# Performance work log

Measured on AMD Instinct MI355X. Metric: run time of the kernel, lower is better.

The kernel has to match this reference:

```python
import jax, jax.numpy as jnp
import numpy as np

N = 50000   # total nodes
E = 100000  # total edges
F = 64      # input node features
H = 128     # hidden_dim
HEADS = 4
B = 64      # number of graphs in the batch
S = 512     # num_stations
LC = 8      # num_line_colors


def setup_inputs() -> dict:
    key = jax.random.key(0)
    ks = jax.random.split(key, 40)
    w = lambda i, shape: (jax.random.normal(ks[i], shape, jnp.float32) * 0.02)
    inp = {
        'node_features': jax.random.normal(ks[0], (N, F), jnp.float32),
        'edge_index': jax.random.randint(ks[1], (2, E), 0, N),
        'batch': jnp.sort(jax.random.randint(ks[2], (N,), 0, B)),
        # initial projection F -> H
        'Wp': w(3, (F, H)), 'bp': w(4, (H,)),
        # TransformerConv 1: in H, out H, heads HEADS (concat)
        'Wq1': w(5, (H, HEADS * H)), 'bq1': w(6, (HEADS * H,)),
        'Wk1': w(7, (H, HEADS * H)), 'bk1': w(8, (HEADS * H,)),
        'Wv1': w(9, (H, HEADS * H)), 'bv1': w(10, (HEADS * H,)),
        'Ws1': w(11, (H, HEADS * H)), 'bs1': w(12, (HEADS * H,)),
        # TransformerConv 2: in HEADS*H, out H, heads 1
        'Wq2': w(13, (HEADS * H, H)), 'bq2': w(14, (H,)),
        'Wk2': w(15, (HEADS * H, H)), 'bk2': w(16, (H,)),
        'Wv2': w(17, (HEADS * H, H)), 'bv2': w(18, (H,)),
        'Ws2': w(19, (HEADS * H, H)), 'bs2': w(20, (H,)),
        # output heads
        'crW': w(21, (H, 1)),  'crb': w(22, (1,)),
        'hlW': w(23, (H, 4)),  'hlb': w(24, (4,)),
        'mtW': w(25, (H, 3)),  'mtb': w(26, (3,)),
        'p1W': w(27, (H, S)),  'p1b': w(28, (S,)),
        'p2W': w(29, (H, S)),  'p2b': w(30, (S,)),
        'dtW': w(31, (H, S)),  'dtb': w(32, (S,)),
        'slW': w(33, (H, LC)), 'slb': w(34, (LC,)),
    }
    return inp


def transformer_conv(x, src, dst, Wq, bq, Wk, bk, Wv, bv, Ws, bs, heads, out_ch):
    # PyG TransformerConv (beta=False, concat=True, root_weight=True):
    #   alpha_ij = softmax_j( (W_q x_i) . (W_k x_j) / sqrt(d) ) over in-edges of i
    #   out_i    = sum_j alpha_ij * (W_v x_j)  (concat heads) + W_skip x_i
    n = x.shape[0]
    q = (x @ Wq + bq).reshape(n, heads, out_ch)
    k = (x @ Wk + bk).reshape(n, heads, out_ch)
    v = (x @ Wv + bv).reshape(n, heads, out_ch)
    scores = jnp.sum(q[dst] * k[src], axis=-1) / jnp.sqrt(jnp.float32(out_ch))  # [E,heads]
    m = jax.ops.segment_max(scores, dst, num_segments=n)                        # per-target max
    e = jnp.exp(scores - m[dst])
    denom = jax.ops.segment_sum(e, dst, num_segments=n)
    alpha = e / (denom[dst] + 1e-16)                                            # [E,heads]
    out = jax.ops.segment_sum(alpha[:, :, None] * v[src], dst, num_segments=n)  # [N,heads,out]
    return out.reshape(n, heads * out_ch) + (x @ Ws + bs)


def reference(node_features, edge_index, batch, Wp, bp,
              Wq1, bq1, Wk1, bk1, Wv1, bv1, Ws1, bs1,
              Wq2, bq2, Wk2, bk2, Wv2, bv2, Ws2, bs2,
              crW, crb, hlW, hlb, mtW, mtb, p1W, p1b, p2W, p2b, dtW, dtb, slW, slb):
    src, dst = edge_index[0], edge_index[1]
    h = jax.nn.relu(node_features @ Wp + bp)
    h = jax.nn.relu(transformer_conv(h, src, dst, Wq1, bq1, Wk1, bk1, Wv1, bv1, Ws1, bs1, HEADS, H))
    h = jax.nn.relu(transformer_conv(h, src, dst, Wq2, bq2, Wk2, bk2, Wv2, bv2, Ws2, bs2, 1, H))
    # global mean pool over graphs
    counts = jax.ops.segment_sum(jnp.ones((h.shape[0],), h.dtype), batch, num_segments=B)
    g = jax.ops.segment_sum(h, batch, num_segments=B) / jnp.maximum(counts, 1.0)[:, None]  # [B,H]
    value = g @ crW + crb
    return (value,
            g @ hlW + hlb,
            g @ mtW + mtb,
            g @ p1W + p1b,
            g @ p2W + p2b,
            g @ dtW + dtb,
            g @ slW + slb)
```

## Files before the change

kernel.cpp:

```cpp
#include <hip/hip_runtime.h>
#include <hip/hip_bf16.h>

#define NN 50000
#define EE 100000
#define FF 64
#define HH 128
#define HEADS 4
#define BB 64
#define SS 512
#define LCC 8
#define DEGCAP 32

__device__ __forceinline__ float b2f(ushort u) {
    return __uint_as_float(((unsigned)u) << 16);
}
__device__ __forceinline__ ushort f2b(float f) {
    unsigned u = __float_as_uint(f);
    unsigned r = (u + 0x7FFFu + ((u >> 16) & 1u)) >> 16;
    return (ushort)r;
}
__device__ __forceinline__ uint f2b_pk(float a, float b) {
    __hip_bfloat162 h = __float22bfloat162_rn(make_float2(a, b));
    return *reinterpret_cast<uint*>(&h);
}

__device__ __forceinline__ uint f2fp8x4(float a, float b, float c, float d) {
    int r = __builtin_amdgcn_cvt_pk_fp8_f32(a, b, 0, false);
    r = __builtin_amdgcn_cvt_pk_fp8_f32(c, d, r, true);
    return (uint)r;
}
__device__ __forceinline__ void fp8x4(uint u, float* f) {
    auto lo = __builtin_amdgcn_cvt_pk_f32_fp8((int)u, false);
    auto hi = __builtin_amdgcn_cvt_pk_f32_fp8((int)u, true);
    f[0] = lo[0]; f[1] = lo[1]; f[2] = hi[0]; f[3] = hi[1];
}
__device__ __forceinline__ unsigned char f2fp8_1(float v) {
    int r = __builtin_amdgcn_cvt_pk_fp8_f32(v, 0.f, 0, false);
    return (unsigned char)(r & 0xFF);
}

typedef __attribute__((ext_vector_type(4))) float f32x4;
typedef __attribute__((ext_vector_type(8))) short s16x8;
typedef __attribute__((ext_vector_type(4))) uint u32x4;

__device__ __forceinline__ void glls16(const ushort* g, ushort* l) {
    __builtin_amdgcn_global_load_lds((const __attribute__((address_space(1))) void*)g,
                                     (__attribute__((address_space(3))) void*)l, 16, 0, 0);
}
__device__ __forceinline__ void glls16b(const unsigned char* g, unsigned char* l) {
    __builtin_amdgcn_global_load_lds((const __attribute__((address_space(1))) void*)g,
                                     (__attribute__((address_space(3))) void*)l, 16, 0, 0);
}

#define BM 128
#define BN 128
#define BK 64
#define EST 68

__global__ __launch_bounds__(512) void gemm_f8(
    const unsigned char* __restrict__ A8, const unsigned char* __restrict__ B8,
    const float* __restrict__ bias,
    ushort* __restrict__ C1,
    unsigned char* __restrict__ D0, unsigned char* __restrict__ D1,
    unsigned char* __restrict__ D2,
    int mode, int M, int K, int gx, int gy)
{
    __shared__ __align__(16) unsigned char Sm[384 * 128];

    const int bid  = blockIdx.x;
    const int xcd  = bid & 7;
    const int slot = bid >> 3;
    const int bx   = slot % gx;
    const int by   = xcd + 8 * (slot / gx);
    if (by >= gy) return;
    const int m0 = by * BM;
    const int n0 = bx * 256;

    const int t = threadIdx.x;
    const int lane = t & 63;
    const int wave = t >> 6;
    const int wm = (wave & 1) * 64;
    const int wn = (wave >> 1) * 64;
    const int lrow = lane & 15;
    const int g    = lane >> 4;

    const int wbase = n0 + wn;
    float bj[4];
#pragma unroll
    for (int j = 0; j < 4; ++j) bj[j] = bias[wbase + j * 16 + lrow];

    const unsigned char* gp[6];
#pragma unroll
    for (int p = 0; p < 6; ++p) {
        const int row = wave * 48 + p * 8 + (lane >> 3);
        const int cg  = ((lane & 7) ^ (row & 7)) << 4;
        gp[p] = (row < 128)
              ? A8 + (size_t)min(m0 + row, M - 1) * K + cg
              : B8 + (size_t)(n0 + row - 128) * K + cg;
    }

    f32x4 acc[4][4];
#pragma unroll
    for (int i = 0; i < 4; ++i)
#pragma unroll
        for (int j = 0; j < 4; ++j)
            acc[i][j] = (f32x4){bj[j], bj[j], bj[j], bj[j]};

    const int sub = ((g & 1) << 3);
    for (int k0 = 0; k0 < K; k0 += 128) {
#pragma unroll
        for (int p = 0; p < 6; ++p)
            glls16b(gp[p] + k0, Sm + (wave * 48 + p * 8) * 128);
        __syncthreads();

#pragma unroll
        for (int kk = 0; kk < 4; ++kk) {
            const int gr = (kk << 1) + (g >> 1);
            long af[4], bf[4];
#pragma unroll
            for (int i = 0; i < 4; ++i) {
                const int R = wm + i * 16 + lrow;
                af[i] = *(const long*)&Sm[(R << 7) + ((gr ^ (R & 7)) << 4) + sub];
            }
#pragma unroll
            for (int j = 0; j < 4; ++j) {
                const int R = wn + j * 16 + lrow;
                bf[j] = *(const long*)&Sm[((128 + R) << 7) + ((gr ^ (R & 7)) << 4) + sub];
            }
#pragma unroll
            for (int i = 0; i < 4; ++i)
#pragma unroll
                for (int j = 0; j < 4; ++j)
                    acc[i][j] = __builtin_amdgcn_mfma_f32_16x16x32_fp8_fp8(af[i], bf[j], acc[i][j], 0, 0, 0);
        }
        __syncthreads();
    }

    float* Es = (float*)Sm + wave * (16 * EST);

    bool bfout = false;
    float os = 0.0625f;
    unsigned char* Cw8 = nullptr; int ldw8 = 0, cb8 = 0;
    if (mode == 1) {
        if (wbase < 512) { Cw8 = D0; ldw8 = 512; cb8 = wbase; }
        else {
            const int u = wbase - 512;
            const int h = u >> 8;
            const int c = u & 255;
            if (c < 128) { Cw8 = D1; ldw8 = 512; cb8 = h * 128 + c; }
            else         { Cw8 = D2; ldw8 = 512; cb8 = h * 128 + (c - 128); }
        }
    } else {
        if (wbase < 128) { bfout = true; os = 1.0f / 256.0f; }
        else { Cw8 = D0; ldw8 = 384; cb8 = wbase - 128; }
    }

    const int rbase = (lane >> 4) * 4;
    const int rrow  = lane >> 2;
    const int rcol  = (lane & 3) << 4;

#pragma unroll
    for (int i = 0; i < 4; ++i) {
#pragma unroll
        for (int j = 0; j < 4; ++j)
#pragma unroll
            for (int r = 0; r < 4; ++r)
                Es[(rbase + r) * EST + j * 16 + lrow] = acc[i][j][r] * os;
        const int gm = m0 + wm + i * 16 + rrow;
        if (gm < M) {
            const float* srcp = Es + rrow * EST + rcol;
            f32x4 f0 = *(const f32x4*)(srcp + 0);
            f32x4 f1 = *(const f32x4*)(srcp + 4);
            f32x4 f2 = *(const f32x4*)(srcp + 8);
            f32x4 f3 = *(const f32x4*)(srcp + 12);
            if (bfout) {
                u32x4 o0, o1;
                o0[0] = f2b_pk(f0[0], f0[1]); o0[1] = f2b_pk(f0[2], f0[3]);
                o0[2] = f2b_pk(f1[0], f1[1]); o0[3] = f2b_pk(f1[2], f1[3]);
                o1[0] = f2b_pk(f2[0], f2[1]); o1[1] = f2b_pk(f2[2], f2[3]);
                o1[2] = f2b_pk(f3[0], f3[1]); o1[3] = f2b_pk(f3[2], f3[3]);
                ushort* dst = C1 + (size_t)gm * 128 + wbase + rcol;
                *(u32x4*)(dst + 0) = o0;
                *(u32x4*)(dst + 8) = o1;
            } else {
                u32x4 o;
                o[0] = f2fp8x4(f0[0], f0[1], f0[2], f0[3]);
                o[1] = f2fp8x4(f1[0], f1[1], f1[2], f1[3]);
                o[2] = f2fp8x4(f2[0], f2[1], f2[2], f2[3]);
                o[3] = f2fp8x4(f3[0], f3[1], f3[2], f3[3]);
                *(u32x4*)(Cw8 + (size_t)gm * ldw8 + cb8 + rcol) = o;
            }
        }
    }
}

__global__ __launch_bounds__(256) void gemm_bf16(
    const ushort* __restrict__ A, const ushort* __restrict__ Bt,
    const float* __restrict__ bias,
    unsigned char* __restrict__ C8,
    int M, int K, int gy)
{
    __shared__ __align__(16) ushort Sm[2 * BM * BK];
    ushort* As = Sm;
    ushort* Bs = Sm + BM * BK;

    const int bid  = blockIdx.x;
    const int xcd  = bid & 7;
    const int by   = xcd + 8 * (bid >> 3);
    if (by >= gy) return;
    const int m0 = by * BM;

    const int t = threadIdx.x;
    const int lane = t & 63;
    const int wave = t >> 6;
    const int wm = (wave & 1) * 64;
    const int wn = (wave >> 1) * 64;
    const int lrow = lane & 15;
    const int g    = lane >> 4;

    const int wbase = wn;
    float bj[4];
#pragma unroll
    for (int j = 0; j < 4; ++j) bj[j] = bias[wbase + j * 16 + lrow];

    const int srow = (wave << 5) + (lane >> 3);
    const int scs  = lane & 7;

    const ushort* ga[4];
    const ushort* gb[4];
#pragma unroll
    for (int p = 0; p < 4; ++p) {
        const int row = srow + (p << 3);
        const int l   = scs ^ (row & 7);
        ga[p] = A + (size_t)min(m0 + row, M - 1) * K + (l << 3);
        gb[p] = Bt + (size_t)row * K + (l << 3);
    }
    const int ldsoff = (wave << 11);

    f32x4 acc[4][4];
#pragma unroll
    for (int i = 0; i < 4; ++i)
#pragma unroll
        for (int j = 0; j < 4; ++j)
            acc[i][j] = (f32x4){bj[j], bj[j], bj[j], bj[j]};

    for (int k0 = 0; k0 < K; k0 += BK) {
#pragma unroll
        for (int p = 0; p < 4; ++p) glls16(ga[p] + k0, As + ldsoff + (p << 9));
#pragma unroll
        for (int p = 0; p < 4; ++p) glls16(gb[p] + k0, Bs + ldsoff + (p << 9));
        __syncthreads();

#pragma unroll
        for (int kk = 0; kk < 2; ++kk) {
            s16x8 af[4], bf[4];
#pragma unroll
            for (int i = 0; i < 4; ++i) {
                const int R = wm + i * 16 + lrow;
                const int c = ((kk << 2) + g) ^ (R & 7);
                af[i] = *(const s16x8*)&As[(R << 6) + (c << 3)];
            }
#pragma unroll
            for (int j = 0; j < 4; ++j) {
                const int R = wn + j * 16 + lrow;
                const int c = ((kk << 2) + g) ^ (R & 7);
                bf[j] = *(const s16x8*)&Bs[(R << 6) + (c << 3)];
            }
#pragma unroll
            for (int i = 0; i < 4; ++i)
#pragma unroll
                for (int j = 0; j < 4; ++j)
                    acc[i][j] = __builtin_amdgcn_mfma_f32_16x16x32_bf16(af[i], bf[j], acc[i][j], 0, 0, 0);
        }
        __syncthreads();
    }

    float* Es = (float*)Sm + wave * (16 * EST);

    const int rbase = (lane >> 4) * 4;
    const int rrow  = lane >> 2;
    const int rcol  = (lane & 3) << 4;

#pragma unroll
    for (int i = 0; i < 4; ++i) {
#pragma unroll
        for (int j = 0; j < 4; ++j)
#pragma unroll
            for (int r = 0; r < 4; ++r)
                Es[(rbase + r) * EST + j * 16 + lrow] = fmaxf(acc[i][j][r], 0.f);
        const int gm = m0 + wm + i * 16 + rrow;
        if (gm < M) {
            const float* srcp = Es + rrow * EST + rcol;
            f32x4 f0 = *(const f32x4*)(srcp + 0);
            f32x4 f1 = *(const f32x4*)(srcp + 4);
            f32x4 f2 = *(const f32x4*)(srcp + 8);
            f32x4 f3 = *(const f32x4*)(srcp + 12);
            u32x4 o;
            o[0] = f2fp8x4(16.f * f0[0], 16.f * f0[1], 16.f * f0[2], 16.f * f0[3]);
            o[1] = f2fp8x4(16.f * f1[0], 16.f * f1[1], 16.f * f1[2], 16.f * f1[3]);
            o[2] = f2fp8x4(16.f * f2[0], 16.f * f2[1], 16.f * f2[2], 16.f * f2[3]);
            o[3] = f2fp8x4(16.f * f3[0], 16.f * f3[1], 16.f * f3[2], 16.f * f3[3]);
            *(u32x4*)(C8 + (size_t)gm * 128 + wbase + rcol) = o;
        }
    }
}

__global__ __launch_bounds__(256) void mcomp_kernel(
    const float* __restrict__ Wq1, const float* __restrict__ Wk1,
    unsigned char* __restrict__ f1w8)
{
    __shared__ float Aq[16][132];
    __shared__ float Bk[16][132];

    const int blk = blockIdx.x;
    const int h  = blk >> 6;
    const int bt = (blk >> 3) & 7;
    const int at = blk & 7;
    const int tid = threadIdx.x;

    const int r  = tid >> 4;
    const int cc = (tid & 15) * 8;
    const float* qrow = Wq1 + (size_t)(at * 16 + r) * 512 + h * 128 + cc;
    const float* krow = Wk1 + (size_t)(bt * 16 + r) * 512 + h * 128 + cc;
#pragma unroll
    for (int j = 0; j < 8; ++j) Aq[r][cc + j] = qrow[j];
#pragma unroll
    for (int j = 0; j < 8; ++j) Bk[r][cc + j] = krow[j];
    __syncthreads();

    const int ta = tid >> 4, tb = tid & 15;
    float acc = 0.f;
#pragma unroll 8
    for (int d = 0; d < 128; ++d) acc += Aq[ta][d] * Bk[tb][d];

    const int a = at * 16 + ta, b = bt * 16 + tb;
    f1w8[(size_t)(512 + h * 256 + b) * 128 + a] = f2fp8_1(acc * 16.0f);
}

#define F1OFF  8192
#define F2OFF  204800
#define WTOTAL 466944
#define BTOT   2048
#define MWORK  (HEADS * 128)
#define CVTN   (NN * FF / 4)

__global__ void prep_kernel(
    const float* __restrict__ nf, ushort* __restrict__ nfb,
    const float* __restrict__ Wp,
    const float* __restrict__ Wq1, const float* __restrict__ Wk1,
    const float* __restrict__ Wv1, const float* __restrict__ Ws1,
    const float* __restrict__ Wq2, const float* __restrict__ Wk2,
    const float* __restrict__ Wv2, const float* __restrict__ Ws2,
    const float* __restrict__ bs1, const float* __restrict__ bq1,
    const float* __restrict__ bv1, const float* __restrict__ bs2,
    const float* __restrict__ bq2, const float* __restrict__ bk2, const float* __restrict__ bv2,
    ushort* __restrict__ wt, unsigned char* __restrict__ f1w8, unsigned char* __restrict__ f2w8,
    float* __restrict__ bb,
    unsigned* __restrict__ zerop, int zn)
{
    int t0 = blockIdx.x * 256 + threadIdx.x;
    if (t0 < CVTN) {
        float4 v = ((const float4*)nf)[t0];
        uint2 o;
        o.x = f2b_pk(v.x, v.y);
        o.y = f2b_pk(v.z, v.w);
        ((uint2*)nfb)[t0] = o;
        return;
    }
    int t = t0 - CVTN;
    if (t < WTOTAL) {
        if (t < F1OFF) {
            int n = t >> 6, k = t & 63;
            wt[t] = f2b(Wp[k * 128 + n]);
        } else if (t < F2OFF) {
            int u = t - F1OFF;
            int n = u >> 7, k = u & 127;
            float v;
            if (n < 512) v = Ws1[k * 512 + n];
            else {
                int r = n - 512;
                int h = r >> 8, c = r & 255;
                if (c < 128) return;
                v = Wv1[k * 512 + h * 128 + (c - 128)];
            }
            f1w8[(size_t)n * 128 + k] = f2fp8_1(v * 16.0f);
        } else {
            int u = t - F2OFF;
            int n = u >> 9, k = u & 511;
            float w;
            if (n < 128) w = Ws2[k * 128 + n];
            else {
                int r = n - 128;
                const float* W = (r < 128) ? Wq2 : (r < 256) ? Wk2 : Wv2;
                w = W[k * 128 + (r & 127)];
            }
            f2w8[(size_t)n * 512 + k] = f2fp8_1(w * 16.0f);
        }
    } else if (t < WTOTAL + BTOT) {
        int u = t - WTOTAL;
        float v;
        if (u < 512) v = bs1[u] * 256.0f;
        else if (u < 1536) {
            int r = u - 512;
            int h = r >> 8, c = r & 255;
            if (c < 128) return;
            v = bv1[h * 128 + (c - 128)] * 256.0f;
        } else {
            int c = u - 1536;
            v = 256.0f * ((c < 128) ? bs2[c]
              : (c < 256) ? bq2[c - 128]
              : (c < 384) ? bk2[c - 256] : bv2[c - 384]);
        }
        bb[u] = v;
    } else if (t < WTOTAL + BTOT + MWORK) {
        int u = t - (WTOTAL + BTOT);
        int h = u >> 7, b = u & 127;
        const float* wk = Wk1 + b * 512 + h * 128;
        const float* bq = bq1 + h * 128;
        float acc = 0.f;
#pragma unroll 8
        for (int d = 0; d < 128; ++d) acc += wk[d] * bq[d];
        bb[512 + h * 256 + b] = acc * 256.0f;
    } else {
        int z = t - (WTOTAL + BTOT + MWORK);
        if (z < zn) zerop[z] = 0u;
    }
}

__global__ void bucket_direct_kernel(const int* __restrict__ src, const int* __restrict__ dst,
                                     int* __restrict__ cnt, int* __restrict__ srcs2, int E)
{
    int e = blockIdx.x * 256 + threadIdx.x;
    if (e >= E) return;
    int d = dst[e];
    int p = atomicAdd(&cnt[d], 1);
    if (p < DEGCAP) srcs2[d * DEGCAP + p] = src[e];
}

__global__ __launch_bounds__(256) void gather4_kernel(
    const unsigned char* __restrict__ Qu, const unsigned char* __restrict__ kq8,
    const unsigned char* __restrict__ v4,
    const int* __restrict__ cnt, const int* __restrict__ srcs2,
    const unsigned char* __restrict__ s8,
    unsigned char* __restrict__ outp, float scale, int n)
{
    int i = blockIdx.x * 4 + (threadIdx.x >> 6);
    int lane = threadIdx.x & 63;
    if (i >= n) return;
    const int h = lane >> 4;
    const int l = lane & 15;
    const int vo = h * 128 + l * 8;

    uint2 uq = *(const uint2*)(Qu + (size_t)i * 512 + h * 128 + l * 8);
    uint2 sk = *(const uint2*)(s8 + (size_t)i * 512 + h * 128 + l * 8);
    float q[8];
    fp8x4(uq.x, q); fp8x4(uq.y, q + 4);

    const int deg = min(cnt[i], DEGCAP);
    const int* rowp = srcs2 + (size_t)i * DEGCAP;
    float den = 0.f;
    float o[8] = {0.f, 0.f, 0.f, 0.f, 0.f, 0.f, 0.f, 0.f};
    int p = 0;
    for (; p + 2 <= deg; p += 2) {
        int s0 = rowp[p], s1 = rowp[p + 1];
        uint2 ka = *(const uint2*)(kq8 + (size_t)s0 * 128 + l * 8);
        uint2 kb = *(const uint2*)(kq8 + (size_t)s1 * 128 + l * 8);
        uint2 va = *(const uint2*)(v4 + (size_t)s0 * 512 + vo);
        uint2 vb = *(const uint2*)(v4 + (size_t)s1 * 512 + vo);
        float kaf[8], kbf[8];
        fp8x4(ka.x, kaf); fp8x4(ka.y, kaf + 4);
        fp8x4(kb.x, kbf); fp8x4(kb.y, kbf + 4);
        float da = 0.f, db = 0.f;
#pragma unroll
        for (int d = 0; d < 8; ++d) {
            da += q[d] * kaf[d];
            db += q[d] * kbf[d];
        }
#pragma unroll
        for (int off = 8; off > 0; off >>= 1) {
            da += __shfl_xor(da, off, 64);
            db += __shfl_xor(db, off, 64);
        }
        float ea = __expf(da * scale);
        float eb = __expf(db * scale);
        den += ea + eb;
        float fa[8], fb[8];
        fp8x4(va.x, fa); fp8x4(va.y, fa + 4);
        fp8x4(vb.x, fb); fp8x4(vb.y, fb + 4);
#pragma unroll
        for (int d = 0; d < 8; ++d) o[d] += ea * fa[d] + eb * fb[d];
    }
    if (p < deg) {
        int s = rowp[p];
        uint2 kv = *(const uint2*)(kq8 + (size_t)s * 128 + l * 8);
        uint2 vv = *(const uint2*)(v4 + (size_t)s * 512 + vo);
        float kf[8];
        fp8x4(kv.x, kf); fp8x4(kv.y, kf + 4);
        float d0 = 0.f;
#pragma unroll
        for (int d = 0; d < 8; ++d) d0 += q[d] * kf[d];
#pragma unroll
        for (int off = 8; off > 0; off >>= 1) d0 += __shfl_xor(d0, off, 64);
        float e = __expf(d0 * scale);
        den += e;
        float fv[8];
        fp8x4(vv.x, fv); fp8x4(vv.y, fv + 4);
#pragma unroll
        for (int d = 0; d < 8; ++d) o[d] += e * fv[d];
    }
    float invd = 1.0f / (den + 1e-16f);
    float skf[8];
    fp8x4(sk.x, skf); fp8x4(sk.y, skf + 4);
    float r[8];
#pragma unroll
    for (int d = 0; d < 8; ++d) r[d] = fmaxf(skf[d] + o[d] * invd, 0.f);
    uint2 ov;
    ov.x = f2fp8x4(r[0], r[1], r[2], r[3]);
    ov.y = f2fp8x4(r[4], r[5], r[6], r[7]);
    *(uint2*)(outp + (size_t)i * 512 + h * 128 + l * 8) = ov;
}

__global__ __launch_bounds__(256) void edge_gather_kernel(
    const unsigned char* __restrict__ qkv,
    const int* __restrict__ cnt, const int* __restrict__ srcs2,
    const ushort* __restrict__ skip,
    ushort* __restrict__ outp, float scale, int n)
{
    int i = blockIdx.x * 4 + (threadIdx.x >> 6);
    int lane = threadIdx.x & 63;
    if (i >= n) return;
    const int g = lane >> 4;
    const int l = lane & 15;

    uint2 uq = *(const uint2*)(qkv + (size_t)i * 384 + l * 8);
    float q[8];
    fp8x4(uq.x, q); fp8x4(uq.y, q + 4);

    const int deg = min(cnt[i], DEGCAP);
    const int* rowp = srcs2 + (size_t)i * DEGCAP;
    float den = 0.f;
    float o[8] = {0.f, 0.f, 0.f, 0.f, 0.f, 0.f, 0.f, 0.f};
    for (int pb = 0; pb < deg; pb += 4) {
        int p = pb + g;
        bool act = p < deg;
        int s = rowp[act ? p : 0];
        const unsigned char* row = qkv + (size_t)s * 384;
        uint2 kv = *(const uint2*)(row + 128 + l * 8);
        uint2 vv = *(const uint2*)(row + 256 + l * 8);
        float kf[8];
        fp8x4(kv.x, kf); fp8x4(kv.y, kf + 4);
        float d0 = 0.f;
#pragma unroll
        for (int d = 0; d < 8; ++d) d0 += q[d] * kf[d];
#pragma unroll
        for (int off = 8; off > 0; off >>= 1) d0 += __shfl_xor(d0, off, 64);
        float e = act ? __expf(d0 * scale) : 0.f;
        den += e;
        float vf[8];
        fp8x4(vv.x, vf); fp8x4(vv.y, vf + 4);
#pragma unroll
        for (int d = 0; d < 8; ++d) o[d] += e * vf[d];
    }
#pragma unroll
    for (int off = 16; off < 64; off <<= 1) {
        den += __shfl_xor(den, off, 64);
#pragma unroll
        for (int d = 0; d < 8; ++d) o[d] += __shfl_xor(o[d], off, 64);
    }
    if (g == 0) {
        float inv = 0.0625f / (den + 1e-16f);
        s16x8 sk = *(const s16x8*)(skip + (size_t)i * 128 + l * 8);
        float r[8];
#pragma unroll
        for (int d = 0; d < 8; ++d) r[d] = b2f((ushort)sk[d]) + o[d] * inv;
        u32x4 ov;
        ov[0] = f2b_pk(r[0], r[1]);
        ov[1] = f2b_pk(r[2], r[3]);
        ov[2] = f2b_pk(r[4], r[5]);
        ov[3] = f2b_pk(r[6], r[7]);
        *(u32x4*)(outp + (size_t)i * 128 + l * 8) = ov;
    }
}

__global__ __launch_bounds__(256) void pool_kernel(
    const ushort* __restrict__ h, const int* __restrict__ batch,
    float* __restrict__ gsum, float* __restrict__ cnt, int n)
{
    int wave = threadIdx.x >> 6, lane = threadIdx.x & 63;
    int start = blockIdx.x * 256 + wave * 64;
    int end = min(start + 64, n);
    if (start >= end) return;
    int cur = batch[start];
    float a0 = 0.f, a1 = 0.f;
    int run = 0;
    for (int node = start; node < end; ++node) {
        int g = batch[node];
        if (g != cur) {
            atomicAdd(&gsum[cur * HH + 2 * lane], a0);
            atomicAdd(&gsum[cur * HH + 2 * lane + 1], a1);
            if (lane == 0) atomicAdd(&cnt[cur], (float)run);
            cur = g; a0 = a1 = 0.f; run = 0;
        }
        uint x = ((const uint*)h)[(size_t)node * 64 + lane];
        a0 += fmaxf(b2f((ushort)x), 0.f);
        a1 += fmaxf(b2f((ushort)(x >> 16)), 0.f);
        ++run;
    }
    atomicAdd(&gsum[cur * HH + 2 * lane], a0);
    atomicAdd(&gsum[cur * HH + 2 * lane + 1], a1);
    if (lane == 0) atomicAdd(&cnt[cur], (float)run);
}

__global__ void out_heads_kernel(
    const float* __restrict__ gsum, const float* __restrict__ cntb,
    const float* __restrict__ w0, const float* __restrict__ b0,
    const float* __restrict__ w1, const float* __restrict__ b1,
    const float* __restrict__ w2, const float* __restrict__ b2,
    const float* __restrict__ w3, const float* __restrict__ b3,
    const float* __restrict__ w4, const float* __restrict__ b4,
    const float* __restrict__ w5, const float* __restrict__ b5,
    const float* __restrict__ w6, const float* __restrict__ b6,
    float* __restrict__ out, int total)
{
    int t = blockIdx.x * blockDim.x + threadIdx.x;
    if (t >= total) return;
    const float* W; const float* bias; int cols; int local;
    if      (t < 64)    { W = w0; bias = b0; cols = 1;   local = t; }
    else if (t < 320)   { W = w1; bias = b1; cols = 4;   local = t - 64; }
    else if (t < 512)   { W = w2; bias = b2; cols = 3;   local = t - 320; }
    else if (t < 33280) { W = w3; bias = b3; cols = SS;  local = t - 512; }
    else if (t < 66048) { W = w4; bias = b4; cols = SS;  local = t - 33280; }
    else if (t < 98816) { W = w5; bias = b5; cols = SS;  local = t - 66048; }
    else                { W = w6; bias = b6; cols = LCC; local = t - 98816; }
    int b = local / cols, c = local % cols;
    const float* gr = gsum + b * HH;
    float inv = 1.0f / fmaxf(cntb[b], 1.0f);
    float s = 0.f;
#pragma unroll 8
    for (int i = 0; i < HH; ++i) s += gr[i] * W[i * cols + c];
    out[t] = bias[c] + s * inv;
}

extern "C" void kernel_launch(void* const* d_in, const int* in_sizes, int n_in,
                              void* d_out, int out_size, void* d_ws, size_t ws_size,
                              hipStream_t stream)
{
    (void)in_sizes; (void)n_in; (void)out_size; (void)ws_size;

    const float* nf   = (const float*)d_in[0];
    const int*   ei   = (const int*)d_in[1];
    const int*   src  = ei;
    const int*   dst  = ei + EE;
    const int*   batch= (const int*)d_in[2];
    const float* Wp   = (const float*)d_in[3];
    const float* bp   = (const float*)d_in[4];
    const float* Wq1  = (const float*)d_in[5];
    const float* bq1  = (const float*)d_in[6];
    const float* Wk1  = (const float*)d_in[7];
    const float* bk1  = (const float*)d_in[8];
    const float* Wv1  = (const float*)d_in[9];
    const float* bv1  = (const float*)d_in[10];
    const float* Ws1  = (const float*)d_in[11];
    const float* bs1  = (const float*)d_in[12];
    const float* Wq2  = (const float*)d_in[13];
    const float* bq2  = (const float*)d_in[14];
    const float* Wk2  = (const float*)d_in[15];
    const float* bk2  = (const float*)d_in[16];
    const float* Wv2  = (const float*)d_in[17];
    const float* bv2  = (const float*)d_in[18];
    const float* Ws2  = (const float*)d_in[19];
    const float* bs2  = (const float*)d_in[20];
    const float* crW  = (const float*)d_in[21];
    const float* crb  = (const float*)d_in[22];
    const float* hlW  = (const float*)d_in[23];
    const float* hlb  = (const float*)d_in[24];
    const float* mtW  = (const float*)d_in[25];
    const float* mtb  = (const float*)d_in[26];
    const float* p1W  = (const float*)d_in[27];
    const float* p1b  = (const float*)d_in[28];
    const float* p2W  = (const float*)d_in[29];
    const float* p2b  = (const float*)d_in[30];
    const float* dtW  = (const float*)d_in[31];
    const float* dtb  = (const float*)d_in[32];
    const float* slW  = (const float*)d_in[33];
    const float* slb  = (const float*)d_in[34];
    float* out = (float*)d_out;

    (void)bk1;

    unsigned char* base = (unsigned char*)d_ws;
    unsigned char* kq8 = base;
    unsigned char* v4  = base + (size_t)NN * 128;
    unsigned char* Qu8 = base + (size_t)NN * 640;
    ushort* h2sb = (ushort*)base;
    unsigned char* qkv8 = base + (size_t)NN * 256;
    ushort* h2   = (ushort*)(base + (size_t)NN * 640);
    unsigned char* s8 = base + (size_t)NN * 1152;
    unsigned char* h1f8 = base + (size_t)NN * 1664;
    ushort* nfb  = (ushort*)h1f8;
    ushort* wt   = (ushort*)(base + (size_t)NN * 2176);
    float*  bb   = (float*)(wt + F1OFF);
    unsigned char* f1w8 = (unsigned char*)(bb + BTOT);
    unsigned char* f2w8 = f1w8 + 1536 * 128;
    int*    srcs2 = (int*)(f2w8 + 512 * 512);
    int*    cnt   = srcs2 + (size_t)NN * DEGCAP;
    float*  gsum  = (float*)(cnt + NN);
    float*  cntb  = gsum + BB * HH;

    const float scale = 0.08838834764831845f;
    const dim3 blk(256);
    const int gy  = (NN + BM - 1) / BM;
    const int gyp = ((gy + 7) / 8) * 8;

    const int filln = NN + BB * HH + BB;
    const int ptot = CVTN + WTOTAL + BTOT + MWORK + filln;
    prep_kernel<<<(ptot + 255) / 256, blk, 0, stream>>>(
        nf, nfb, Wp, Wq1, Wk1, Wv1, Ws1, Wq2, Wk2, Wv2, Ws2,
        bs1, bq1, bv1, bs2, bq2, bk2, bv2, wt, f1w8, f2w8, bb, (unsigned*)cnt, filln);

    mcomp_kernel<<<dim3(256), blk, 0, stream>>>(Wq1, Wk1, f1w8);

    bucket_direct_kernel<<<(EE + 255) / 256, blk, 0, stream>>>(src, dst, cnt, srcs2, EE);

    gemm_bf16<<<dim3(gyp), blk, 0, stream>>>(
        nfb, wt, bp, kq8, NN, FF, gy);

    gemm_f8<<<dim3(6 * gyp), dim3(512), 0, stream>>>(
        kq8, f1w8, bb, nullptr, s8, Qu8, v4, 1, NN, 128, 6, gy);

    gather4_kernel<<<(NN + 3) / 4, blk, 0, stream>>>(
        Qu8, kq8, v4, cnt, srcs2, s8, h1f8, scale * 0.00390625f, NN);

    gemm_f8<<<dim3(2 * gyp), dim3(512), 0, stream>>>(
        h1f8, f2w8, bb + 1536, h2sb, qkv8, nullptr, nullptr, 2, NN, 512, 2, gy);

    edge_gather_kernel<<<(NN + 3) / 4, blk, 0, stream>>>(
        qkv8, cnt, srcs2, h2sb, h2, scale * 0.00390625f, NN);

    pool_kernel<<<(NN + 255) / 256, blk, 0, stream>>>(h2, batch, gsum, cntb, NN);

    const int total = BB * (1 + 4 + 3 + SS + SS + SS + LCC);
    out_heads_kernel<<<(total + 255) / 256, blk, 0, stream>>>(
        gsum, cntb, crW, crb, hlW, hlb, mtW, mtb, p1W, p1b, p2W, p2b, dtW, dtb, slW, slb, out, total);
}
```

Measured before the change: 286.7 us.

## Fuse input projection GEMM into first-layer FP8 GEMM and merge mcomp into prep

The bf16 input projection (F->H with ReLU) is now computed inside each first-layer FP8 GEMM block. Its output is quantized straight into shared memory as the A tile, and only the bx==0 blocks write kq8 back to global memory. The separate mcomp kernel becomes extra blocks of the prep kernel, which saves launches. In exchange, the projection is recomputed six times per row tile, once per column block, and half the waves sit idle during that phase.

```diff
diff --git a/kernel.cpp b/kernel.cpp
--- a/kernel.cpp
+++ b/kernel.cpp
@@ -43,35 +43,204 @@
 typedef __attribute__((ext_vector_type(8))) short s16x8;
 typedef __attribute__((ext_vector_type(4))) uint u32x4;
 
-__device__ __forceinline__ void glls16(const ushort* g, ushort* l) {
-    __builtin_amdgcn_global_load_lds((const __attribute__((address_space(1))) void*)g,
-                                     (__attribute__((address_space(3))) void*)l, 16, 0, 0);
-}
 __device__ __forceinline__ void glls16b(const unsigned char* g, unsigned char* l) {
     __builtin_amdgcn_global_load_lds((const __attribute__((address_space(1))) void*)g,
                                      (__attribute__((address_space(3))) void*)l, 16, 0, 0);
 }
 
 #define BM 128
-#define BN 128
-#define BK 64
 #define EST 68
 
-__global__ __launch_bounds__(512) void gemm_f8(
-    const unsigned char* __restrict__ A8, const unsigned char* __restrict__ B8,
-    const float* __restrict__ bias,
-    ushort* __restrict__ C1,
+__global__ __launch_bounds__(512) void f1_fused(
+    const ushort* __restrict__ nfb, const ushort* __restrict__ wpt,
+    const float* __restrict__ bp,
+    const unsigned char* __restrict__ B8, const float* __restrict__ bias,
+    unsigned char* __restrict__ kq8,
     unsigned char* __restrict__ D0, unsigned char* __restrict__ D1,
     unsigned char* __restrict__ D2,
-    int mode, int M, int K, int gx, int gy)
+    int M, int gy)
 {
     __shared__ __align__(16) unsigned char Sm[384 * 128];
 
     const int bid  = blockIdx.x;
     const int xcd  = bid & 7;
     const int slot = bid >> 3;
-    const int bx   = slot % gx;
-    const int by   = xcd + 8 * (slot / gx);
+    const int bx   = slot % 6;
+    const int by   = xcd + 8 * (slot / 6);
+    if (by >= gy) return;
+    const int m0 = by * BM;
+    const int n0 = bx * 256;
+
+    const int t = threadIdx.x;
+    const int lane = t & 63;
+    const int wave = t >> 6;
+    const int lrow = lane & 15;
+    const int g    = lane >> 4;
+
+    f32x4 acc[4][4];
+
+    if (wave < 4) {
+        const int wmP = (wave & 1) * 64;
+        const int wnP = (wave >> 1) * 64;
+        float bpj[4];
+#pragma unroll
+        for (int j = 0; j < 4; ++j) bpj[j] = bp[wnP + j * 16 + lrow];
+#pragma unroll
+        for (int i = 0; i < 4; ++i)
+#pragma unroll
+            for (int j = 0; j < 4; ++j)
+                acc[i][j] = (f32x4){bpj[j], bpj[j], bpj[j], bpj[j]};
+
+        s16x8 afp[4][2], bfp[4][2];
+#pragma unroll
+        for (int i = 0; i < 4; ++i) {
+            const size_t ar = (size_t)min(m0 + wmP + i * 16 + lrow, M - 1) * 64;
+#pragma unroll
+            for (int kk = 0; kk < 2; ++kk)
+                afp[i][kk] = *(const s16x8*)&nfb[ar + ((kk << 2) + g) * 8];
+        }
+#pragma unroll
+        for (int j = 0; j < 4; ++j) {
+            const size_t br = (size_t)(wnP + j * 16 + lrow) * 64;
+#pragma unroll
+            for (int kk = 0; kk < 2; ++kk)
+                bfp[j][kk] = *(const s16x8*)&wpt[br + ((kk << 2) + g) * 8];
+        }
+#pragma unroll
+        for (int kk = 0; kk < 2; ++kk)
+#pragma unroll
+            for (int i = 0; i < 4; ++i)
+#pragma unroll
+                for (int j = 0; j < 4; ++j)
+                    acc[i][j] = __builtin_amdgcn_mfma_f32_16x16x32_bf16(afp[i][kk], bfp[j][kk], acc[i][j], 0, 0, 0);
+
+#pragma unroll
+        for (int i = 0; i < 4; ++i)
+#pragma unroll
+            for (int j = 0; j < 4; ++j) {
+                const int c = wnP + j * 16 + lrow;
+                const int R0 = wmP + i * 16 + g * 4;
+#pragma unroll
+                for (int r = 0; r < 4; ++r) {
+                    const int R = R0 + r;
+                    const float v = fmaxf(acc[i][j][r], 0.f) * 16.0f;
+                    Sm[(R << 7) + ((((c >> 4)) ^ (R & 7)) << 4) + (c & 15)] = f2fp8_1(v);
+                }
+            }
+    } else {
+        const int br = (wave - 4) * 64;
+#pragma unroll
+        for (int p = 0; p < 8; ++p) {
+            const int rloc = br + p * 8 + (lane >> 3);
+            const int cg   = ((lane & 7) ^ (rloc & 7)) << 4;
+            glls16b(B8 + (size_t)(n0 + rloc) * 128 + cg,
+                    Sm + (size_t)(128 + br + p * 8) * 128);
+        }
+    }
+    __syncthreads();
+
+    const int wm = (wave & 1) * 64;
+    const int wn = (wave >> 1) * 64;
+    const int wbase = n0 + wn;
+    {
+        float bj[4];
+#pragma unroll
+        for (int j = 0; j < 4; ++j) bj[j] = bias[wbase + j * 16 + lrow];
+#pragma unroll
+        for (int i = 0; i < 4; ++i)
+#pragma unroll
+            for (int j = 0; j < 4; ++j)
+                acc[i][j] = (f32x4){bj[j], bj[j], bj[j], bj[j]};
+    }
+
+    const int sub = ((g & 1) << 3);
+#pragma unroll
+    for (int kk = 0; kk < 4; ++kk) {
+        const int gr = (kk << 1) + (g >> 1);
+        long af[4], bf[4];
+#pragma unroll
+        for (int i = 0; i < 4; ++i) {
+            const int R = wm + i * 16 + lrow;
+            af[i] = *(const long*)&Sm[(R << 7) + ((gr ^ (R & 7)) << 4) + sub];
+        }
+#pragma unroll
+        for (int j = 0; j < 4; ++j) {
+            const int R = wn + j * 16 + lrow;
+            bf[j] = *(const long*)&Sm[((128 + R) << 7) + ((gr ^ (R & 7)) << 4) + sub];
+        }
+#pragma unroll
+        for (int i = 0; i < 4; ++i)
+#pragma unroll
+            for (int j = 0; j < 4; ++j)
+                acc[i][j] = __builtin_amdgcn_mfma_f32_16x16x32_fp8_fp8(af[i], bf[j], acc[i][j], 0, 0, 0);
+    }
+    __syncthreads();
+
+    if (bx == 0) {
+        for (int idx = t; idx < 1024; idx += 512) {
+            const int row = idx >> 3, gr8 = idx & 7;
+            const int gm = m0 + row;
+            if (gm < M) {
+                u32x4 v = *(const u32x4*)&Sm[(row << 7) + ((gr8 ^ (row & 7)) << 4)];
+                *(u32x4*)(kq8 + (size_t)gm * 128 + gr8 * 16) = v;
+            }
+        }
+    }
+    __syncthreads();
+
+    float* Es = (float*)Sm + wave * (16 * EST);
+
+    unsigned char* Cw8; int ldw8, cb8;
+    if (wbase < 512) { Cw8 = D0; ldw8 = 512; cb8 = wbase; }
+    else {
+        const int u = wbase - 512;
+        const int h = u >> 8;
+        const int c = u & 255;
+        if (c < 128) { Cw8 = D1; ldw8 = 512; cb8 = h * 128 + c; }
+        else         { Cw8 = D2; ldw8 = 512; cb8 = h * 128 + (c - 128); }
+    }
+
+    const int rbase = g * 4;
+    const int rrow  = lane >> 2;
+    const int rcol  = (lane & 3) << 4;
+
+#pragma unroll
+    for (int i = 0; i < 4; ++i) {
+#pragma unroll
+        for (int j = 0; j < 4; ++j)
+#pragma unroll
+            for (int r = 0; r < 4; ++r)
+                Es[(rbase + r) * EST + j * 16 + lrow] = acc[i][j][r] * 0.0625f;
+        const int gm = m0 + wm + i * 16 + rrow;
+        if (gm < M) {
+            const float* srcp = Es + rrow * EST + rcol;
+            f32x4 f0 = *(const f32x4*)(srcp + 0);
+            f32x4 f1 = *(const f32x4*)(srcp + 4);
+            f32x4 f2 = *(const f32x4*)(srcp + 8);
+            f32x4 f3 = *(const f32x4*)(srcp + 12);
+            u32x4 o;
+            o[0] = f2fp8x4(f0[0], f0[1], f0[2], f0[3]);
+            o[1] = f2fp8x4(f1[0], f1[1], f1[2], f1[3]);
+            o[2] = f2fp8x4(f2[0], f2[1], f2[2], f2[3]);
+            o[3] = f2fp8x4(f3[0], f3[1], f3[2], f3[3]);
+            *(u32x4*)(Cw8 + (size_t)gm * ldw8 + cb8 + rcol) = o;
+        }
+    }
+}
+
+__global__ __launch_bounds__(512) void gemm_f2(
+    const unsigned char* __restrict__ A8, const unsigned char* __restrict__ B8,
+    const float* __restrict__ bias,
+    ushort* __restrict__ h2sb, unsigned char* __restrict__ qkv8,
+    int M, int gy)
+{
+    __shared__ __align__(16) unsigned char Sm[384 * 128];
+
+    const int bid  = blockIdx.x;
+    const int xcd  = bid & 7;
+    const int slot = bid >> 3;
+    const int bx   = slot % 2;
+    const int by   = xcd + 8 * (slot / 2);
     if (by >= gy) return;
     const int m0 = by * BM;
     const int n0 = bx * 256;
@@ -95,8 +264,8 @@
         const int row = wave * 48 + p * 8 + (lane >> 3);
         const int cg  = ((lane & 7) ^ (row & 7)) << 4;
         gp[p] = (row < 128)
-              ? A8 + (size_t)min(m0 + row, M - 1) * K + cg
-              : B8 + (size_t)(n0 + row - 128) * K + cg;
+              ? A8 + (size_t)min(m0 + row, M - 1) * 512 + cg
+              : B8 + (size_t)(n0 + row - 128) * 512 + cg;
     }
 
     f32x4 acc[4][4];
@@ -107,7 +276,7 @@
             acc[i][j] = (f32x4){bj[j], bj[j], bj[j], bj[j]};
 
     const int sub = ((g & 1) << 3);
-    for (int k0 = 0; k0 < K; k0 += 128) {
+    for (int k0 = 0; k0 < 512; k0 += 128) {
 #pragma unroll
         for (int p = 0; p < 6; ++p)
             glls16b(gp[p] + k0, Sm + (wave * 48 + p * 8) * 128);
@@ -138,24 +307,10 @@
 
     float* Es = (float*)Sm + wave * (16 * EST);
 
-    bool bfout = false;
-    float os = 0.0625f;
-    unsigned char* Cw8 = nullptr; int ldw8 = 0, cb8 = 0;
-    if (mode == 1) {
-        if (wbase < 512) { Cw8 = D0; ldw8 = 512; cb8 = wbase; }
-        else {
-            const int u = wbase - 512;
-            const int h = u >> 8;
-            const int c = u & 255;
-            if (c < 128) { Cw8 = D1; ldw8 = 512; cb8 = h * 128 + c; }
-            else         { Cw8 = D2; ldw8 = 512; cb8 = h * 128 + (c - 128); }
-        }
-    } else {
-        if (wbase < 128) { bfout = true; os = 1.0f / 256.0f; }
-        else { Cw8 = D0; ldw8 = 384; cb8 = wbase - 128; }
-    }
-
-    const int rbase = (lane >> 4) * 4;
+    const bool skipw = (wbase < 128);
+    const float os = skipw ? (1.0f / 256.0f) : 0.0625f;
+
+    const int rbase = g * 4;
     const int rrow  = lane >> 2;
     const int rcol  = (lane & 3) << 4;
 
@@ -173,13 +328,13 @@
             f32x4 f1 = *(const f32x4*)(srcp + 4);
             f32x4 f2 = *(const f32x4*)(srcp + 8);
             f32x4 f3 = *(const f32x4*)(srcp + 12);
-            if (bfout) {
+            if (skipw) {
                 u32x4 o0, o1;
                 o0[0] = f2b_pk(f0[0], f0[1]); o0[1] = f2b_pk(f0[2], f0[3]);
                 o0[2] = f2b_pk(f1[0], f1[1]); o0[3] = f2b_pk(f1[2], f1[3]);
                 o1[0] = f2b_pk(f2[0], f2[1]); o1[1] = f2b_pk(f2[2], f2[3]);
                 o1[2] = f2b_pk(f3[0], f3[1]); o1[3] = f2b_pk(f3[2], f3[3]);
-                ushort* dst = C1 + (size_t)gm * 128 + wbase + rcol;
+                ushort* dst = h2sb + (size_t)gm * 128 + wbase + rcol;
                 *(u32x4*)(dst + 0) = o0;
                 *(u32x4*)(dst + 8) = o1;
             } else {
@@ -188,153 +343,10 @@
                 o[1] = f2fp8x4(f1[0], f1[1], f1[2], f1[3]);
                 o[2] = f2fp8x4(f2[0], f2[1], f2[2], f2[3]);
                 o[3] = f2fp8x4(f3[0], f3[1], f3[2], f3[3]);
-                *(u32x4*)(Cw8 + (size_t)gm * ldw8 + cb8 + rcol) = o;
+                *(u32x4*)(qkv8 + (size_t)gm * 384 + (wbase - 128) + rcol) = o;
             }
         }
     }
-}
-
-__global__ __launch_bounds__(256) void gemm_bf16(
-    const ushort* __restrict__ A, const ushort* __restrict__ Bt,
-    const float* __restrict__ bias,
-    unsigned char* __restrict__ C8,
-    int M, int K, int gy)
-{
-    __shared__ __align__(16) ushort Sm[2 * BM * BK];
-    ushort* As = Sm;
-    ushort* Bs = Sm + BM * BK;
-
-    const int bid  = blockIdx.x;
-    const int xcd  = bid & 7;
-    const int by   = xcd + 8 * (bid >> 3);
-    if (by >= gy) return;
-    const int m0 = by * BM;
-
-    const int t = threadIdx.x;
-    const int lane = t & 63;
-    const int wave = t >> 6;
-    const int wm = (wave & 1) * 64;
-    const int wn = (wave >> 1) * 64;
-    const int lrow = lane & 15;
-    const int g    = lane >> 4;
-
-    const int wbase = wn;
-    float bj[4];
-#pragma unroll
-    for (int j = 0; j < 4; ++j) bj[j] = bias[wbase + j * 16 + lrow];
-
-    const int srow = (wave << 5) + (lane >> 3);
-    const int scs  = lane & 7;
-
-    const ushort* ga[4];
-    const ushort* gb[4];
-#pragma unroll
-    for (int p = 0; p < 4; ++p) {
-        const int row = srow + (p << 3);
-        const int l   = scs ^ (row & 7);
-        ga[p] = A + (size_t)min(m0 + row, M - 1) * K + (l << 3);
-        gb[p] = Bt + (size_t)row * K + (l << 3);
-    }
-    const int ldsoff = (wave << 11);
-
-    f32x4 acc[4][4];
-#pragma unroll
-    for (int i = 0; i < 4; ++i)
-#pragma unroll
-        for (int j = 0; j < 4; ++j)
-            acc[i][j] = (f32x4){bj[j], bj[j], bj[j], bj[j]};
-
-    for (int k0 = 0; k0 < K; k0 += BK) {
-#pragma unroll
-        for (int p = 0; p < 4; ++p) glls16(ga[p] + k0, As + ldsoff + (p << 9));
-#pragma unroll
-        for (int p = 0; p < 4; ++p) glls16(gb[p] + k0, Bs + ldsoff + (p << 9));
-        __syncthreads();
-
-#pragma unroll
-        for (int kk = 0; kk < 2; ++kk) {
-            s16x8 af[4], bf[4];
-#pragma unroll
-            for (int i = 0; i < 4; ++i) {
-                const int R = wm + i * 16 + lrow;
-                const int c = ((kk << 2) + g) ^ (R & 7);
-                af[i] = *(const s16x8*)&As[(R << 6) + (c << 3)];
-            }
-#pragma unroll
-            for (int j = 0; j < 4; ++j) {
-                const int R = wn + j * 16 + lrow;
-                const int c = ((kk << 2) + g) ^ (R & 7);
-                bf[j] = *(const s16x8*)&Bs[(R << 6) + (c << 3)];
-            }
-#pragma unroll
-            for (int i = 0; i < 4; ++i)
-#pragma unroll
-                for (int j = 0; j < 4; ++j)
-                    acc[i][j] = __builtin_amdgcn_mfma_f32_16x16x32_bf16(af[i], bf[j], acc[i][j], 0, 0, 0);
-        }
-        __syncthreads();
-    }
-
-    float* Es = (float*)Sm + wave * (16 * EST);
-
-    const int rbase = (lane >> 4) * 4;
-    const int rrow  = lane >> 2;
-    const int rcol  = (lane & 3) << 4;
-
-#pragma unroll
-    for (int i = 0; i < 4; ++i) {
-#pragma unroll
-        for (int j = 0; j < 4; ++j)
-#pragma unroll
-            for (int r = 0; r < 4; ++r)
-                Es[(rbase + r) * EST + j * 16 + lrow] = fmaxf(acc[i][j][r], 0.f);
-        const int gm = m0 + wm + i * 16 + rrow;
-        if (gm < M) {
-            const float* srcp = Es + rrow * EST + rcol;
-            f32x4 f0 = *(const f32x4*)(srcp + 0);
-            f32x4 f1 = *(const f32x4*)(srcp + 4);
-            f32x4 f2 = *(const f32x4*)(srcp + 8);
-            f32x4 f3 = *(const f32x4*)(srcp + 12);
-            u32x4 o;
-            o[0] = f2fp8x4(16.f * f0[0], 16.f * f0[1], 16.f * f0[2], 16.f * f0[3]);
-            o[1] = f2fp8x4(16.f * f1[0], 16.f * f1[1], 16.f * f1[2], 16.f * f1[3]);
-            o[2] = f2fp8x4(16.f * f2[0], 16.f * f2[1], 16.f * f2[2], 16.f * f2[3]);
-            o[3] = f2fp8x4(16.f * f3[0], 16.f * f3[1], 16.f * f3[2], 16.f * f3[3]);
-            *(u32x4*)(C8 + (size_t)gm * 128 + wbase + rcol) = o;
-        }
-    }
-}
-
-__global__ __launch_bounds__(256) void mcomp_kernel(
-    const float* __restrict__ Wq1, const float* __restrict__ Wk1,
-    unsigned char* __restrict__ f1w8)
-{
-    __shared__ float Aq[16][132];
-    __shared__ float Bk[16][132];
-
-    const int blk = blockIdx.x;
-    const int h  = blk >> 6;
-    const int bt = (blk >> 3) & 7;
-    const int at = blk & 7;
-    const int tid = threadIdx.x;
-
-    const int r  = tid >> 4;
-    const int cc = (tid & 15) * 8;
-    const float* qrow = Wq1 + (size_t)(at * 16 + r) * 512 + h * 128 + cc;
-    const float* krow = Wk1 + (size_t)(bt * 16 + r) * 512 + h * 128 + cc;
-#pragma unroll
-    for (int j = 0; j < 8; ++j) Aq[r][cc + j] = qrow[j];
-#pragma unroll
-    for (int j = 0; j < 8; ++j) Bk[r][cc + j] = krow[j];
-    __syncthreads();
-
-    const int ta = tid >> 4, tb = tid & 15;
-    float acc = 0.f;
-#pragma unroll 8
-    for (int d = 0; d < 128; ++d) acc += Aq[ta][d] * Bk[tb][d];
-
-    const int a = at * 16 + ta, b = bt * 16 + tb;
-    f1w8[(size_t)(512 + h * 256 + b) * 128 + a] = f2fp8_1(acc * 16.0f);
 }
 
 #define F1OFF  8192
@@ -356,8 +368,38 @@
     const float* __restrict__ bq2, const float* __restrict__ bk2, const float* __restrict__ bv2,
     ushort* __restrict__ wt, unsigned char* __restrict__ f1w8, unsigned char* __restrict__ f2w8,
     float* __restrict__ bb,
-    unsigned* __restrict__ zerop, int zn)
-{
+    unsigned* __restrict__ zerop, int zn, int pblocks)
+{
+    __shared__ float Aq[16][132];
+    __shared__ float Bk[16][132];
+
+    if ((int)blockIdx.x >= pblocks) {
+        const int blk = blockIdx.x - pblocks;
+        const int h  = blk >> 6;
+        const int bt = (blk >> 3) & 7;
+        const int at = blk & 7;
+        const int tid = threadIdx.x;
+
+        const int r  = tid >> 4;
+        const int cc = (tid & 15) * 8;
+        const float* qrow = Wq1 + (size_t)(at * 16 + r) * 512 + h * 128 + cc;
+        const float* krow = Wk1 + (size_t)(bt * 16 + r) * 512 + h * 128 + cc;
+#pragma unroll
+        for (int j = 0; j < 8; ++j) Aq[r][cc + j] = qrow[j];
+#pragma unroll
+        for (int j = 0; j < 8; ++j) Bk[r][cc + j] = krow[j];
+        __syncthreads();
+
+        const int ta = tid >> 4, tb = tid & 15;
+        float acc = 0.f;
+#pragma unroll 8
+        for (int d = 0; d < 128; ++d) acc += Aq[ta][d] * Bk[tb][d];
+
+        const int a = at * 16 + ta, b = bt * 16 + tb;
+        f1w8[(size_t)(512 + h * 256 + b) * 128 + a] = f2fp8_1(acc * 16.0f);
+        return;
+    }
+
     int t0 = blockIdx.x * 256 + threadIdx.x;
     if (t0 < CVTN) {
         float4 v = ((const float4*)nf)[t0];
@@ -714,25 +756,21 @@
 
     const int filln = NN + BB * HH + BB;
     const int ptot = CVTN + WTOTAL + BTOT + MWORK + filln;
-    prep_kernel<<<(ptot + 255) / 256, blk, 0, stream>>>(
+    const int pblocks = (ptot + 255) / 256;
+    prep_kernel<<<pblocks + 256, blk, 0, stream>>>(
         nf, nfb, Wp, Wq1, Wk1, Wv1, Ws1, Wq2, Wk2, Wv2, Ws2,
-        bs1, bq1, bv1, bs2, bq2, bk2, bv2, wt, f1w8, f2w8, bb, (unsigned*)cnt, filln);
-
-    mcomp_kernel<<<dim3(256), blk, 0, stream>>>(Wq1, Wk1, f1w8);
+        bs1, bq1, bv1, bs2, bq2, bk2, bv2, wt, f1w8, f2w8, bb, (unsigned*)cnt, filln, pblocks);
 
     bucket_direct_kernel<<<(EE + 255) / 256, blk, 0, stream>>>(src, dst, cnt, srcs2, EE);
 
-    gemm_bf16<<<dim3(gyp), blk, 0, stream>>>(
-        nfb, wt, bp, kq8, NN, FF, gy);
-
-    gemm_f8<<<dim3(6 * gyp), dim3(512), 0, stream>>>(
-        kq8, f1w8, bb, nullptr, s8, Qu8, v4, 1, NN, 128, 6, gy);
+    f1_fused<<<dim3(6 * gyp), dim3(512), 0, stream>>>(
+        nfb, wt, bp, f1w8, bb, kq8, s8, Qu8, v4, NN, gy);
 
     gather4_kernel<<<(NN + 3) / 4, blk, 0, stream>>>(
         Qu8, kq8, v4, cnt, srcs2, s8, h1f8, scale * 0.00390625f, NN);
 
-    gemm_f8<<<dim3(2 * gyp), dim3(512), 0, stream>>>(
-        h1f8, f2w8, bb + 1536, h2sb, qkv8, nullptr, nullptr, 2, NN, 512, 2, gy);
+    gemm_f2<<<dim3(2 * gyp), dim3(512), 0, stream>>>(
+        h1f8, f2w8, bb + 1536, h2sb, qkv8, NN, gy);
 
     edge_gather_kernel<<<(NN + 3) / 4, blk, 0, stream>>>(
         qkv8, cnt, srcs2, h2sb, h2, scale * 0.00390625f, NN);
```

New measurement: 317.4 us. 10.7% more time.
